# Performance work log

Hardware: AMD Instinct MI355X
Metric: run time of the kernel (lower is better)

The kernel has to match this reference:

```python
import jax, jax.numpy as jnp
import numpy as np

UNITS = 1024
IN_DIM = 1024
BATCH = 8192


def setup_inputs() -> dict:
    key = jax.random.key(0)
    ks = jax.random.split(key, 8)
    return {
        "inputs": jax.random.normal(ks[0], (BATCH, IN_DIM), dtype=jnp.float32),
        "c_prev": jax.random.normal(ks[1], (BATCH, UNITS), dtype=jnp.float32),
        "h_prev": jax.random.normal(ks[2], (BATCH, UNITS), dtype=jnp.float32),
        "kernel": jax.random.normal(ks[3], (IN_DIM, 4 * UNITS), dtype=jnp.float32) * 0.02,
        "recurrent_kernel": jax.random.normal(ks[4], (UNITS, 4 * UNITS), dtype=jnp.float32) * 0.02,
        "bias": jnp.zeros((4 * UNITS,), dtype=jnp.float32),
        "peephole_f": jax.random.normal(ks[5], (UNITS,), dtype=jnp.float32) * 0.1,
        "peephole_i": jax.random.normal(ks[6], (UNITS,), dtype=jnp.float32) * 0.1,
        "peephole_o": jax.random.normal(ks[7], (UNITS,), dtype=jnp.float32) * 0.1,
    }


def reference(inputs, c_prev, h_prev, kernel, recurrent_kernel, bias,
              peephole_f, peephole_i, peephole_o):
    # z: [B, 4U] = x @ W + h_prev @ U + b
    z = inputs @ kernel + h_prev @ recurrent_kernel + bias
    z_f, z_i, z_c, z_o = jnp.split(z, 4, axis=1)
    f = jax.nn.sigmoid(z_f + peephole_f * c_prev)
    i = jax.nn.sigmoid(z_i + peephole_i * c_prev)
    c_tilde = jnp.tanh(z_c)
    c = f * c_prev + i * c_tilde
    o = jax.nn.sigmoid(z_o + peephole_o * c)
    h = o * jnp.tanh(c)
    return h, c
```

## Files before the change

### kernel.cpp

```cpp
#include <hip/hip_runtime.h>

typedef unsigned short u16;
typedef __attribute__((ext_vector_type(8))) short bf16x8;
typedef __attribute__((ext_vector_type(4))) float f32x4;

constexpr int BATCH = 8192;
constexpr int UNITS = 1024;
constexpr int K2    = 2048;
constexpr int N4    = 4096;
constexpr int BK    = 64;
constexpr int BM    = 256;
constexpr int BN    = 256;
constexpr int NKT   = K2 / BK;
constexpr int ASZ   = BM * BK;
constexpr int BSZ   = BN * BK;

__device__ __forceinline__ u16 f2bf(float f) {
  unsigned u = __float_as_uint(f);
  u += 0x7fffu + ((u >> 16) & 1u);
  return (u16)(u >> 16);
}

__device__ __forceinline__ void async_copy16(const void* g, void* l) {
  __builtin_amdgcn_global_load_lds(
      (const __attribute__((address_space(1))) void*)g,
      (__attribute__((address_space(3))) void*)l, 16, 0, 0);
}

__global__ __launch_bounds__(256) void cast_fused_kernel(
    const float* __restrict__ x, const float* __restrict__ h,
    const float* __restrict__ W, const float* __restrict__ U,
    u16* __restrict__ A, u16* __restrict__ B) {
  const int tid = threadIdx.x;
  if (blockIdx.x < 2048) {
    __shared__ float lds[64 * 69];
    const int bid = blockIdx.x;
    const int nb  = bid & 63;
    const int kb  = bid >> 6;
    const int n0  = nb * 64;
    const int k0  = kb * 64;
    const int jn  = n0 >> 10;
    const int q0  = (n0 & 1023) >> 4;
    const float* src = (k0 < UNITS) ? (W + (size_t)k0 * N4)
                                    : (U + (size_t)(k0 - UNITS) * N4);
    {
      const int kk  = tid >> 4;
      const int nn4 = (tid & 15) * 4;
#pragma unroll
      for (int r = 0; r < 4; ++r) {
        const int k = kk + r * 16;
        float4 v = *reinterpret_cast<const float4*>(&src[(size_t)k * N4 + n0 + nn4]);
        lds[k * 69 + nn4 + 0] = v.x;
        lds[k * 69 + nn4 + 1] = v.y;
        lds[k * 69 + nn4 + 2] = v.z;
        lds[k * 69 + nn4 + 3] = v.w;
      }
    }
    __syncthreads();
    {
      const int kk4 = (tid & 15) * 4;
#pragma unroll
      for (int pass = 0; pass < 4; ++pass) {
        const int rr  = (tid >> 4) + pass * 16;
        const int q   = q0 + (rr >> 4);
        const int low = rr & 15;
        const int p   = q * 64 + jn * 16 + low;
        union { ushort4 u4; u16 s[4]; } o;
#pragma unroll
        for (int j = 0; j < 4; ++j) o.s[j] = f2bf(lds[(kk4 + j) * 69 + rr]);
        *reinterpret_cast<ushort4*>(&B[(size_t)p * K2 + k0 + kk4]) = o.u4;
      }
    }
  } else {
    const int t0 = (blockIdx.x - 2048) * 256 + tid;
    const int stride = 4096 * 256;
#pragma unroll
    for (int s = 0; s < 4; ++s) {
      const int g = t0 + s * stride;
      const int idx = g * 4;
      const int b = idx >> 11;
      const int k = idx & 2047;
      const float* src = (k < UNITS) ? (x + (size_t)b * UNITS + k)
                                     : (h + (size_t)b * UNITS + (k - UNITS));
      float4 v = *reinterpret_cast<const float4*>(src);
      union { ushort4 u4; u16 sv[4]; } o;
      o.sv[0] = f2bf(v.x); o.sv[1] = f2bf(v.y);
      o.sv[2] = f2bf(v.z); o.sv[3] = f2bf(v.w);
      *reinterpret_cast<ushort4*>(A + idx) = o.u4;
    }
  }
}

__global__ __launch_bounds__(512, 2) void lstm_gemm_kernel(
    const u16* __restrict__ A, const u16* __restrict__ B,
    const float* __restrict__ bias, const float* __restrict__ c_prev,
    const float* __restrict__ pf, const float* __restrict__ pi,
    const float* __restrict__ po,
    float* __restrict__ out_h, float* __restrict__ out_c) {
  __shared__ u16 lds[3 * ASZ + 2 * BSZ];
  u16* const Asb = lds;
  u16* const Bsb = lds + 3 * ASZ;

  const int tid  = threadIdx.x;
  const int lane = tid & 63;
  const int wave = tid >> 6;
  const int quad = lane >> 4;
  const int c    = lane & 15;

  int lin = blockIdx.y * 16 + blockIdx.x;
  lin = (lin & 7) * 64 + (lin >> 3);
  const int m0 = (lin >> 4) * BM;
  const int n0 = (lin & 15) * BN;

  const int wm = (wave >> 2) * 128;
  const int wn = (wave & 3) * 64;

  const int g8   = ((tid & 7) ^ ((tid >> 3) & 7)) * 8;
  const int rowa = tid >> 3;
  const u16* gA = A + (size_t)(m0 + rowa) * K2 + g8;
  const u16* gB = B + (size_t)(n0 + rowa) * K2 + g8;
  const int ldst = tid * 8;

  const int sl0   = (quad ^ (c & 7)) * 8;
  const int sl1   = ((4 + quad) ^ (c & 7)) * 8;
  const int aoff0 = (wm + c) * 64 + sl0;
  const int aoff1 = (wm + c) * 64 + sl1;
  const int boff0 = (wn + c) * 64 + sl0;
  const int boff1 = (wn + c) * 64 + sl1;

  f32x4 acc[8][4] = {};

#pragma unroll
  for (int i = 0; i < 4; ++i)
    async_copy16(gA + (size_t)i * 64 * K2, &Asb[i * 4096 + ldst]);
#pragma unroll
  for (int i = 0; i < 4; ++i)
    async_copy16(gB + (size_t)i * 64 * K2, &Bsb[i * 4096 + ldst]);
#pragma unroll
  for (int i = 0; i < 4; ++i)
    async_copy16(gA + (size_t)i * 64 * K2 + BK, &Asb[ASZ + i * 4096 + ldst]);
  asm volatile("s_waitcnt vmcnt(4)" ::: "memory");
  __builtin_amdgcn_s_barrier();

  int curA = 0;
#pragma unroll 2
  for (int kt = 0; kt < NKT; ++kt) {
    const u16* as = &Asb[curA * ASZ];
    const u16* bs = &Bsb[(kt & 1) * BSZ];
    const int stgA = (curA == 0) ? 2 : curA - 1;
    u16* sA = &Asb[stgA * ASZ];
    u16* sB = &Bsb[((kt + 1) & 1) * BSZ];
    const bool doB = (kt < NKT - 1);
    const bool doA = (kt < NKT - 2);
    const size_t okB = (size_t)(kt + 1) * BK;
    const size_t okA = (size_t)(kt + 2) * BK;

    bf16x8 bfr[2][4];
#pragma unroll
    for (int ph = 0; ph < 4; ++ph) {
      if (ph == 0 && doB) {
        async_copy16(gB + okB,                     sB + ldst);
        async_copy16(gB + okB + (size_t)64 * K2,   sB + 4096 + ldst);
      }
      if (ph == 1 && doB) {
        async_copy16(gB + okB + (size_t)128 * K2,  sB + 8192 + ldst);
        async_copy16(gB + okB + (size_t)192 * K2,  sB + 12288 + ldst);
      }
      if (ph == 2 && doA) {
        async_copy16(gA + okA,                     sA + ldst);
        async_copy16(gA + okA + (size_t)64 * K2,   sA + 4096 + ldst);
      }
      if (ph == 3 && doA) {
        async_copy16(gA + okA + (size_t)128 * K2,  sA + 8192 + ldst);
        async_copy16(gA + okA + (size_t)192 * K2,  sA + 12288 + ldst);
      }
      if (ph == 0) {
#pragma unroll
        for (int jn = 0; jn < 4; ++jn) {
          bfr[0][jn] = *(const bf16x8*)(bs + boff0 + jn * 1024);
          bfr[1][jn] = *(const bf16x8*)(bs + boff1 + jn * 1024);
        }
      }
      bf16x8 af0[2], af1[2];
#pragma unroll
      for (int jm = 0; jm < 2; ++jm) {
        af0[jm] = *(const bf16x8*)(as + aoff0 + (2 * ph + jm) * 1024);
        af1[jm] = *(const bf16x8*)(as + aoff1 + (2 * ph + jm) * 1024);
      }
      if (ph == 3) {
        if (kt < NKT - 2)       asm volatile("s_waitcnt vmcnt(4)" ::: "memory");
        else if (kt == NKT - 2) asm volatile("s_waitcnt vmcnt(0)" ::: "memory");
      }
      __builtin_amdgcn_s_barrier();
      __builtin_amdgcn_s_setprio(1);
#pragma unroll
      for (int jm = 0; jm < 2; ++jm)
#pragma unroll
        for (int jn = 0; jn < 4; ++jn)
          acc[2 * ph + jm][jn] = __builtin_amdgcn_mfma_f32_16x16x32_bf16(
              af0[jm], bfr[0][jn], acc[2 * ph + jm][jn], 0, 0, 0);
#pragma unroll
      for (int jm = 0; jm < 2; ++jm)
#pragma unroll
        for (int jn = 0; jn < 4; ++jn)
          acc[2 * ph + jm][jn] = __builtin_amdgcn_mfma_f32_16x16x32_bf16(
              af1[jm], bfr[1][jn], acc[2 * ph + jm][jn], 0, 0, 0);
      __builtin_amdgcn_s_setprio(0);
      if (!(ph == 3 && kt == NKT - 1)) {
        __builtin_amdgcn_s_barrier();
      }
    }
    curA = (curA == 2) ? 0 : curA + 1;
  }

  const int u = ((n0 + wn) >> 2) + c;
  const float bf_ = bias[u];
  const float bi_ = bias[UNITS + u];
  const float bc_ = bias[2 * UNITS + u];
  const float bo_ = bias[3 * UNITS + u];
  const float pfv = pf[u], piv = pi[u], pov = po[u];
  const int mbase = m0 + wm + quad * 4;
#pragma unroll
  for (int jm = 0; jm < 8; ++jm) {
#pragma unroll
    for (int r = 0; r < 4; ++r) {
      const int b = mbase + jm * 16 + r;
      const float cp = c_prev[(size_t)b * UNITS + u];
      const float zf = acc[jm][0][r] + bf_ + pfv * cp;
      const float zi = acc[jm][1][r] + bi_ + piv * cp;
      const float zc = acc[jm][2][r] + bc_;
      const float zo = acc[jm][3][r] + bo_;
      const float fg = 1.f / (1.f + __expf(-zf));
      const float ig = 1.f / (1.f + __expf(-zi));
      const float ct = 1.f - 2.f / (__expf(2.f * zc) + 1.f);
      const float cn = fg * cp + ig * ct;
      const float og = 1.f / (1.f + __expf(-(zo + pov * cn)));
      const float hn = og * (1.f - 2.f / (__expf(2.f * cn) + 1.f));
      out_h[(size_t)b * UNITS + u] = hn;
      out_c[(size_t)b * UNITS + u] = cn;
    }
  }
}

extern "C" void kernel_launch(void* const* d_in, const int* in_sizes, int n_in,
                              void* d_out, int out_size, void* d_ws, size_t ws_size,
                              hipStream_t stream) {
  const float* x      = (const float*)d_in[0];
  const float* c_prev = (const float*)d_in[1];
  const float* h_prev = (const float*)d_in[2];
  const float* W      = (const float*)d_in[3];
  const float* U      = (const float*)d_in[4];
  const float* bias   = (const float*)d_in[5];
  const float* pf     = (const float*)d_in[6];
  const float* pi     = (const float*)d_in[7];
  const float* po     = (const float*)d_in[8];
  float* out_h = (float*)d_out;
  float* out_c = out_h + (size_t)BATCH * UNITS;

  u16* Abf = (u16*)d_ws;
  u16* Bbf = Abf + (size_t)BATCH * K2;

  cast_fused_kernel<<<6144, 256, 0, stream>>>(x, h_prev, W, U, Abf, Bbf);
  lstm_gemm_kernel<<<dim3(N4 / BN, BATCH / BM), 512, 0, stream>>>(
      Abf, Bbf, bias, c_prev, pf, pi, po, out_h, out_c);
}
```

Baseline: 160.4 us.

## Switch GEMM mainloop to double-buffered tiles with one barrier per K-step

Replaces the 3-stage A / 2-stage B LDS pipeline, which issued loads and synchronised at every quarter-phase, with a plain double buffer. The next K-tile of both A and B is issued at the start of each iteration, and each iteration ends with a single full vmcnt(0) wait and barrier. A-fragment reads from LDS are now register double-buffered across the four phases so they overlap the MFMAs. This cuts LDS use and the number of barriers, but the global load gets less lead time and the vmcnt(0) wait can expose memory latency.

```diff
diff --git a/kernel.cpp b/kernel.cpp
--- a/kernel.cpp
+++ b/kernel.cpp
@@ -97,9 +97,9 @@
     const float* __restrict__ pf, const float* __restrict__ pi,
     const float* __restrict__ po,
     float* __restrict__ out_h, float* __restrict__ out_c) {
-  __shared__ u16 lds[3 * ASZ + 2 * BSZ];
+  __shared__ u16 lds[2 * ASZ + 2 * BSZ];
   u16* const Asb = lds;
-  u16* const Bsb = lds + 3 * ASZ;
+  u16* const Bsb = lds + 2 * ASZ;
 
   const int tid  = threadIdx.x;
   const int lane = tid & 63;
@@ -131,86 +131,75 @@
   f32x4 acc[8][4] = {};
 
 #pragma unroll
-  for (int i = 0; i < 4; ++i)
+  for (int i = 0; i < 4; ++i) {
     async_copy16(gA + (size_t)i * 64 * K2, &Asb[i * 4096 + ldst]);
-#pragma unroll
-  for (int i = 0; i < 4; ++i)
     async_copy16(gB + (size_t)i * 64 * K2, &Bsb[i * 4096 + ldst]);
-#pragma unroll
-  for (int i = 0; i < 4; ++i)
-    async_copy16(gA + (size_t)i * 64 * K2 + BK, &Asb[ASZ + i * 4096 + ldst]);
-  asm volatile("s_waitcnt vmcnt(4)" ::: "memory");
+  }
+  asm volatile("s_waitcnt vmcnt(0)" ::: "memory");
   __builtin_amdgcn_s_barrier();
-
-  int curA = 0;
+  asm volatile("" ::: "memory");
+
 #pragma unroll 2
   for (int kt = 0; kt < NKT; ++kt) {
-    const u16* as = &Asb[curA * ASZ];
+    const u16* as = &Asb[(kt & 1) * ASZ];
     const u16* bs = &Bsb[(kt & 1) * BSZ];
-    const int stgA = (curA == 0) ? 2 : curA - 1;
-    u16* sA = &Asb[stgA * ASZ];
-    u16* sB = &Bsb[((kt + 1) & 1) * BSZ];
-    const bool doB = (kt < NKT - 1);
-    const bool doA = (kt < NKT - 2);
-    const size_t okB = (size_t)(kt + 1) * BK;
-    const size_t okA = (size_t)(kt + 2) * BK;
+
+    if (kt < NKT - 1) {
+      u16* sA = &Asb[((kt + 1) & 1) * ASZ];
+      u16* sB = &Bsb[((kt + 1) & 1) * BSZ];
+      const size_t ok = (size_t)(kt + 1) * BK;
+#pragma unroll
+      for (int i = 0; i < 4; ++i) {
+        async_copy16(gA + ok + (size_t)i * 64 * K2, sA + i * 4096 + ldst);
+        async_copy16(gB + ok + (size_t)i * 64 * K2, sB + i * 4096 + ldst);
+      }
+    }
 
     bf16x8 bfr[2][4];
 #pragma unroll
+    for (int jn = 0; jn < 4; ++jn) {
+      bfr[0][jn] = *(const bf16x8*)(bs + boff0 + jn * 1024);
+      bfr[1][jn] = *(const bf16x8*)(bs + boff1 + jn * 1024);
+    }
+
+    bf16x8 areg[2][2][2];
+#pragma unroll
+    for (int h = 0; h < 2; ++h)
+#pragma unroll
+      for (int jm = 0; jm < 2; ++jm)
+        areg[0][h][jm] = *(const bf16x8*)(as + (h ? aoff1 : aoff0) + jm * 1024);
+
+#pragma unroll
     for (int ph = 0; ph < 4; ++ph) {
-      if (ph == 0 && doB) {
-        async_copy16(gB + okB,                     sB + ldst);
-        async_copy16(gB + okB + (size_t)64 * K2,   sB + 4096 + ldst);
-      }
-      if (ph == 1 && doB) {
-        async_copy16(gB + okB + (size_t)128 * K2,  sB + 8192 + ldst);
-        async_copy16(gB + okB + (size_t)192 * K2,  sB + 12288 + ldst);
-      }
-      if (ph == 2 && doA) {
-        async_copy16(gA + okA,                     sA + ldst);
-        async_copy16(gA + okA + (size_t)64 * K2,   sA + 4096 + ldst);
-      }
-      if (ph == 3 && doA) {
-        async_copy16(gA + okA + (size_t)128 * K2,  sA + 8192 + ldst);
-        async_copy16(gA + okA + (size_t)192 * K2,  sA + 12288 + ldst);
-      }
-      if (ph == 0) {
-#pragma unroll
-        for (int jn = 0; jn < 4; ++jn) {
-          bfr[0][jn] = *(const bf16x8*)(bs + boff0 + jn * 1024);
-          bfr[1][jn] = *(const bf16x8*)(bs + boff1 + jn * 1024);
-        }
-      }
-      bf16x8 af0[2], af1[2];
-#pragma unroll
-      for (int jm = 0; jm < 2; ++jm) {
-        af0[jm] = *(const bf16x8*)(as + aoff0 + (2 * ph + jm) * 1024);
-        af1[jm] = *(const bf16x8*)(as + aoff1 + (2 * ph + jm) * 1024);
-      }
-      if (ph == 3) {
-        if (kt < NKT - 2)       asm volatile("s_waitcnt vmcnt(4)" ::: "memory");
-        else if (kt == NKT - 2) asm volatile("s_waitcnt vmcnt(0)" ::: "memory");
-      }
-      __builtin_amdgcn_s_barrier();
+      if (ph < 3) {
+#pragma unroll
+        for (int h = 0; h < 2; ++h)
+#pragma unroll
+          for (int jm = 0; jm < 2; ++jm)
+            areg[(ph + 1) & 1][h][jm] = *(const bf16x8*)(
+                as + (h ? aoff1 : aoff0) + (2 * (ph + 1) + jm) * 1024);
+      }
       __builtin_amdgcn_s_setprio(1);
 #pragma unroll
       for (int jm = 0; jm < 2; ++jm)
 #pragma unroll
         for (int jn = 0; jn < 4; ++jn)
           acc[2 * ph + jm][jn] = __builtin_amdgcn_mfma_f32_16x16x32_bf16(
-              af0[jm], bfr[0][jn], acc[2 * ph + jm][jn], 0, 0, 0);
+              areg[ph & 1][0][jm], bfr[0][jn], acc[2 * ph + jm][jn], 0, 0, 0);
 #pragma unroll
       for (int jm = 0; jm < 2; ++jm)
 #pragma unroll
         for (int jn = 0; jn < 4; ++jn)
           acc[2 * ph + jm][jn] = __builtin_amdgcn_mfma_f32_16x16x32_bf16(
-              af1[jm], bfr[1][jn], acc[2 * ph + jm][jn], 0, 0, 0);
+              areg[ph & 1][1][jm], bfr[1][jn], acc[2 * ph + jm][jn], 0, 0, 0);
       __builtin_amdgcn_s_setprio(0);
-      if (!(ph == 3 && kt == NKT - 1)) {
-        __builtin_amdgcn_s_barrier();
-      }
-    }
-    curA = (curA == 2) ? 0 : curA + 1;
+    }
+
+    if (kt < NKT - 1) {
+      asm volatile("s_waitcnt vmcnt(0)" ::: "memory");
+      __builtin_amdgcn_s_barrier();
+      asm volatile("" ::: "memory");
+    }
   }
 
   const int u = ((n0 + wn) >> 2) + c;
```

Measured after the change: 155.3 us, median of 2. 3.2% less time.
